# Optimization experiments

Hardware: AMD Instinct MI355X
Metric: run time of the kernel (lower is better)

Reference implementation:

```python
import jax, jax.numpy as jnp
import numpy as np
from jax import lax

B, C, D, H, W = 2, 1, 128, 128, 128
CONSCIOUSNESS_WEIGHT = 0.1


def _field(depth, height, width, dtype):
    # sin(2*pi*(d+h+w)/(D+H+W)) broadcast over batch/channel
    d = jnp.arange(depth, dtype=dtype)[:, None, None]
    h = jnp.arange(height, dtype=dtype)[None, :, None]
    w = jnp.arange(width, dtype=dtype)[None, None, :]
    phase = 2.0 * jnp.pi * (d + h + w) / (depth + height + width)
    return jnp.sin(phase)  # [D,H,W]


def _conv3d(x, w, b):
    y = lax.conv_general_dilated(
        x, w, window_strides=(1, 1, 1), padding='SAME',
        dimension_numbers=('NCDHW', 'OIDHW', 'NCDHW'))
    return y + b[None, :, None, None, None]


def setup_inputs() -> dict:
    key = jax.random.key(0)
    ks = jax.random.split(key, 4)
    fan1 = 1 * 27
    fan2 = 8 * 27
    fan3 = 16 * 27
    return {
        'cube_data': jax.random.normal(ks[0], (B, C, D, H, W), dtype=jnp.float32),
        'w1': jax.random.normal(ks[1], (8, 1, 3, 3, 3), dtype=jnp.float32) / np.sqrt(fan1),
        'b1': jnp.zeros((8,), dtype=jnp.float32),
        'w2': jax.random.normal(ks[2], (16, 8, 3, 3, 3), dtype=jnp.float32) / np.sqrt(fan2),
        'b2': jnp.zeros((16,), dtype=jnp.float32),
        'w3': jax.random.normal(ks[3], (1, 16, 3, 3, 3), dtype=jnp.float32) / np.sqrt(fan3),
        'b3': jnp.zeros((1,), dtype=jnp.float32),
    }


def reference(cube_data, w1, b1, w2, b2, w3, b3):
    _, _, d, h, w = cube_data.shape
    field = _field(d, h, w, cube_data.dtype)[None, None]  # [1,1,D,H,W]
    integrated = cube_data * (1.0 + CONSCIOUSNESS_WEIGHT * field)
    x = jax.nn.relu(_conv3d(integrated, w1, b1))
    x = jax.nn.relu(_conv3d(x, w2, b2))
    x = jnp.tanh(_conv3d(x, w3, b3))
    return x
```

## Files before the change

### kernel.cpp

```cpp
#include <hip/hip_runtime.h>
#include <hip/hip_fp16.h>

#define VOX (128 * 128 * 128)
#define P 130
#define PP (P * P)
#define PVOX (P * P * P)

typedef unsigned short u16;
typedef _Float16 f16x2 __attribute__((ext_vector_type(2)));
typedef _Float16 f16x8 __attribute__((ext_vector_type(8)));
typedef __attribute__((ext_vector_type(4))) float f32x4;
typedef __attribute__((ext_vector_type(2))) float f32x2;

__device__ __forceinline__ u16 f2h(float f) {
    return __builtin_bit_cast(unsigned short, (_Float16)f);
}
__device__ __forceinline__ unsigned pkh_relu(float a, float b) {
    float ra = a > 0.f ? a : 0.f, rb = b > 0.f ? b : 0.f;
    return (unsigned)f2h(ra) | ((unsigned)f2h(rb) << 16);
}
__device__ __forceinline__ f16x2 h2(unsigned u) { return __builtin_bit_cast(f16x2, u); }

__device__ __forceinline__ float dot2(unsigned a, unsigned b, float c) {
#if __has_builtin(__builtin_amdgcn_fdot2)
    return __builtin_amdgcn_fdot2(h2(a), h2(b), c, false);
#else
    f16x2 av = h2(a), bv = h2(b);
    c = fmaf((float)av.x, (float)bv.x, c);
    return fmaf((float)av.y, (float)bv.y, c);
#endif
}

__device__ __forceinline__ float fast_tanh(float x) {
    float e = __expf(2.0f * x);
    return 1.0f - 2.0f * __builtin_amdgcn_rcpf(1.0f + e);
}

__global__ __launch_bounds__(256) void prep_kernel(
    const float* __restrict__ w1, const float* __restrict__ w2,
    const float* __restrict__ w3, u16* __restrict__ w2frag,
    unsigned* __restrict__ w3p, float2* __restrict__ w1p) {
    int i = blockIdx.x * 256 + threadIdx.x;
    if (i < 3584) {
        int j = i & 7, l = (i >> 3) & 63, s = i >> 9;
        int tap = s * 4 + (l >> 4), oc = l & 15, ic = j;
        float v = (tap < 27) ? w2[(oc * 8 + ic) * 27 + tap] : 0.0f;
        w2frag[i] = f2h(v);
    }
    if (i < 216) {
        int tap = i >> 3, j = i & 7;
        w3p[i] = (unsigned)f2h(w3[(2 * j) * 27 + tap]) |
                 ((unsigned)f2h(w3[(2 * j + 1) * 27 + tap]) << 16);
    }
    if (i < 108) {
        int tap = i >> 2, j = i & 3;
        w1p[i] = make_float2(w1[(2 * j) * 27 + tap], w1[(2 * j + 1) * 27 + tap]);
    }
}

__global__ __launch_bounds__(256) void zero_halo_kernel(u16* __restrict__ x1,
                                                        u16* __restrict__ x2) {
    int i = blockIdx.x * 256 + threadIdx.x;
    if (i >= PVOX) return;
    int d = i / PP;
    int r = i - d * PP;
    int h = r / P;
    int w = r - h * P;
    if (d == 0 || d == P - 1 || h == 0 || h == P - 1 || w == 0 || w == P - 1) {
        uint4 z = {0u, 0u, 0u, 0u};
        *(uint4*)(x1 + (size_t)i * 8) = z;
        *(uint4*)(x2 + (size_t)i * 16) = z;
        *(uint4*)(x2 + (size_t)i * 16 + 8) = z;
    }
}

__global__ __launch_bounds__(256) void integrate_kernel(
    const float* __restrict__ in, u16* __restrict__ x0) {
    int i = blockIdx.x * 256 + threadIdx.x;
    if (i >= PVOX) return;
    int d = i / PP;
    int r = i - d * PP;
    int h = r / P;
    int w = r - h * P;
    float v = 0.0f;
    if (d >= 1 && d <= 128 && h >= 1 && h <= 128 && w >= 1 && w <= 128) {
        int s = (d - 1) + (h - 1) + (w - 1);
        float fld = 1.0f + 0.1f * sinf(6.283185307179586f * (float)s / 384.0f);
        v = in[(size_t)(d - 1) * 16384 + (h - 1) * 128 + (w - 1)] * fld;
    }
    x0[i] = f2h(v);
}

__global__ __launch_bounds__(256) void conv1_kernel(
    const u16* __restrict__ x0, const float2* __restrict__ w1p,
    const float* __restrict__ b1, u16* __restrict__ x1) {
    const int t = blockIdx.x * 256 + threadIdx.x;
    const int w0 = (t & 63) * 2;
    const int h0 = ((t >> 6) & 31) * 4;
    const int d = t >> 11;

    f32x2 acc[4][4][2];
#pragma unroll
    for (int j = 0; j < 4; ++j) {
        const f32x2 b = {b1[2 * j], b1[2 * j + 1]};
#pragma unroll
        for (int i = 0; i < 4; ++i) { acc[i][j][0] = b; acc[i][j][1] = b; }
    }

#pragma unroll
    for (int dz = 0; dz < 3; ++dz) {
        const u16* zb = x0 + (size_t)(d + dz) * PP + (size_t)h0 * P + w0;
        const float2* wz = w1p + dz * 9 * 4;
#pragma unroll
        for (int r = 0; r < 6; ++r) {
            const u16* rp = zb + r * P;
            const unsigned u0 = *(const unsigned*)rp;
            const unsigned u1 = *(const unsigned*)(rp + 2);
            float vv[4];
            vv[0] = (float)h2(u0).x; vv[1] = (float)h2(u0).y;
            vv[2] = (float)h2(u1).x; vv[3] = (float)h2(u1).y;
#pragma unroll
            for (int dy = 0; dy < 3; ++dy) {
                const int i = r - dy;
                if (i < 0 || i > 3) continue;
#pragma unroll
                for (int dx = 0; dx < 3; ++dx) {
                    const f32x2 s0 = {vv[dx], vv[dx]};
                    const f32x2 s1 = {vv[dx + 1], vv[dx + 1]};
#pragma unroll
                    for (int j = 0; j < 4; ++j) {
                        const float2 wraw = wz[(dy * 3 + dx) * 4 + j];
                        const f32x2 wv = {wraw.x, wraw.y};
                        acc[i][j][0] = __builtin_elementwise_fma(wv, s0, acc[i][j][0]);
                        acc[i][j][1] = __builtin_elementwise_fma(wv, s1, acc[i][j][1]);
                    }
                }
            }
        }
    }
    const size_t e0 = ((size_t)(d + 1) * P + (h0 + 1)) * P + (w0 + 1);
#pragma unroll
    for (int i = 0; i < 4; ++i) {
        uint4 oA, oB;
        oA.x = pkh_relu(acc[i][0][0].x, acc[i][0][0].y);
        oA.y = pkh_relu(acc[i][1][0].x, acc[i][1][0].y);
        oA.z = pkh_relu(acc[i][2][0].x, acc[i][2][0].y);
        oA.w = pkh_relu(acc[i][3][0].x, acc[i][3][0].y);
        oB.x = pkh_relu(acc[i][0][1].x, acc[i][0][1].y);
        oB.y = pkh_relu(acc[i][1][1].x, acc[i][1][1].y);
        oB.z = pkh_relu(acc[i][2][1].x, acc[i][2][1].y);
        oB.w = pkh_relu(acc[i][3][1].x, acc[i][3][1].y);
        *(uint4*)(x1 + (e0 + (size_t)i * P) * 8) = oA;
        *(uint4*)(x1 + (e0 + (size_t)i * P + 1) * 8) = oB;
    }
}

__global__ __launch_bounds__(256) void conv2_mfma_kernel(
    const u16* __restrict__ x1, const u16* __restrict__ w2frag,
    const float* __restrict__ b2, u16* __restrict__ x2) {
    const int lane = threadIdx.x & 63;
    const int row = blockIdx.x * 4 + (threadIdx.x >> 6);
    const int q = lane >> 4;
    const int mi = lane & 15;
    const int d0 = row >> 7;
    const int h0 = row & 127;

    f32x4 acc[8];
#pragma unroll
    for (int t = 0; t < 8; ++t) acc[t] = (f32x4){0.f, 0.f, 0.f, 0.f};

#pragma unroll
    for (int s = 0; s < 7; ++s) {
        int tap = s * 4 + q;
        if (tap > 26) tap = 26;
        const int dz = tap / 9;
        const int rem = tap - dz * 9;
        const int dy = rem / 3;
        const int dx = rem - dy * 3;
        const u16* bp = x1 + ((size_t)((d0 + dz) * P + (h0 + dy)) * P + (mi + dx)) * 8;
        const f16x8 wf = *(const f16x8*)(w2frag + (size_t)(s * 64 + lane) * 8);
#pragma unroll
        for (int t = 0; t < 8; ++t) {
            f16x8 act = *(const f16x8*)(bp + t * 128);
            acc[t] = __builtin_amdgcn_mfma_f32_16x16x32_f16(wf, act, acc[t], 0, 0, 0);
        }
    }

    const float4 bv = *(const float4*)(b2 + q * 4);
    const size_t obase = ((size_t)(d0 + 1) * P + (h0 + 1)) * P + 1;
#pragma unroll
    for (int t = 0; t < 8; ++t) {
        const float v0 = acc[t][0] + bv.x;
        const float v1 = acc[t][1] + bv.y;
        const float v2 = acc[t][2] + bv.z;
        const float v3 = acc[t][3] + bv.w;
        uint2 o;
        o.x = pkh_relu(v0, v1);
        o.y = pkh_relu(v2, v3);
        *(uint2*)(x2 + (obase + 16 * t + mi) * 16 + q * 4) = o;
    }
}

__global__ __launch_bounds__(256) void conv3_kernel(
    const u16* __restrict__ x2, const unsigned* __restrict__ w3p,
    const float* __restrict__ b3, float* __restrict__ out) {
    const int t = blockIdx.x * 256 + threadIdx.x;
    const int w = t & 127;
    const int h0 = ((t >> 7) & 15) * 8;
    const int d = t >> 11;

    float accA[8], accB[8];
#pragma unroll
    for (int i = 0; i < 8; ++i) { accA[i] = 0.f; accB[i] = 0.f; }

#pragma unroll 1
    for (int dz = 0; dz < 3; ++dz) {
        const u16* zb = x2 + ((size_t)((d + dz) * P + h0) * P + w) * 16;
        const unsigned* wz = w3p + dz * 9 * 8;
#pragma unroll
        for (int r = 0; r < 10; ++r) {
            const u16* rp = zb + (size_t)r * (P * 16);
            const uint4 c0l = *(const uint4*)(rp);
            const uint4 c0h = *(const uint4*)(rp + 8);
            const uint4 c1l = *(const uint4*)(rp + 16);
            const uint4 c1h = *(const uint4*)(rp + 24);
            const uint4 c2l = *(const uint4*)(rp + 32);
            const uint4 c2h = *(const uint4*)(rp + 40);
#pragma unroll
            for (int dy = 0; dy < 3; ++dy) {
                const int i = r - dy;
                if (i < 0 || i > 7) continue;
                const unsigned* wp = wz + dy * 3 * 8;
                float a = accA[i], b = accB[i];
                a = dot2(c0l.x, wp[0], a);  b = dot2(c0l.y, wp[1], b);
                a = dot2(c0l.z, wp[2], a);  b = dot2(c0l.w, wp[3], b);
                a = dot2(c0h.x, wp[4], a);  b = dot2(c0h.y, wp[5], b);
                a = dot2(c0h.z, wp[6], a);  b = dot2(c0h.w, wp[7], b);
                a = dot2(c1l.x, wp[8], a);  b = dot2(c1l.y, wp[9], b);
                a = dot2(c1l.z, wp[10], a); b = dot2(c1l.w, wp[11], b);
                a = dot2(c1h.x, wp[12], a); b = dot2(c1h.y, wp[13], b);
                a = dot2(c1h.z, wp[14], a); b = dot2(c1h.w, wp[15], b);
                a = dot2(c2l.x, wp[16], a); b = dot2(c2l.y, wp[17], b);
                a = dot2(c2l.z, wp[18], a); b = dot2(c2l.w, wp[19], b);
                a = dot2(c2h.x, wp[20], a); b = dot2(c2h.y, wp[21], b);
                a = dot2(c2h.z, wp[22], a); b = dot2(c2h.w, wp[23], b);
                accA[i] = a; accB[i] = b;
            }
        }
    }
    const float bias = b3[0];
    const size_t obase = (size_t)(d * 128 + h0) * 128 + w;
#pragma unroll
    for (int i = 0; i < 8; ++i)
        out[obase + (size_t)i * 128] = fast_tanh(accA[i] + accB[i] + bias);
}

extern "C" void kernel_launch(void* const* d_in, const int* in_sizes, int n_in,
                              void* d_out, int out_size, void* d_ws, size_t ws_size,
                              hipStream_t stream) {
    const float* cube = (const float*)d_in[0];
    const float* w1 = (const float*)d_in[1];
    const float* b1 = (const float*)d_in[2];
    const float* w2 = (const float*)d_in[3];
    const float* b2 = (const float*)d_in[4];
    const float* w3 = (const float*)d_in[5];
    const float* b3 = (const float*)d_in[6];
    float* out = (float*)d_out;

    char* ws = (char*)d_ws;
    u16* w2frag = (u16*)ws;
    unsigned* w3p = (unsigned*)(ws + 7168);
    float2* w1p = (float2*)(ws + 8032);
    u16* x0 = (u16*)(ws + 16384);
    u16* x1 = (u16*)(ws + 16384 + (size_t)PVOX * sizeof(u16));
    u16* x2 = (u16*)(ws + 16384 + (size_t)PVOX * sizeof(u16) + (size_t)PVOX * 8 * sizeof(u16));

    prep_kernel<<<dim3(14), dim3(256), 0, stream>>>(w1, w2, w3, w2frag, w3p, w1p);
    zero_halo_kernel<<<dim3((PVOX + 255) / 256), dim3(256), 0, stream>>>(x1, x2);

    for (int b = 0; b < 2; ++b) {
        integrate_kernel<<<dim3((PVOX + 255) / 256), dim3(256), 0, stream>>>(
            cube + (size_t)b * VOX, x0);
        conv1_kernel<<<dim3(VOX / 8 / 256), dim3(256), 0, stream>>>(x0, w1p, b1, x1);
        conv2_mfma_kernel<<<dim3(128 * 128 / 4), dim3(256), 0, stream>>>(x1, w2frag, b2, x2);
        conv3_kernel<<<dim3(VOX / 8 / 256), dim3(256), 0, stream>>>(
            x2, w3p, b3, out + (size_t)b * VOX);
    }
}
```

Measured before the change: 264.0 us.

## Share activation loads across dx taps in conv2 MFMA and two depths in conv3

conv2 now runs one MFMA per dx weight fragment on the same activation load, grouping the taps by (dz,dy) into 3 steps instead of 7. The dx-shifted partial sums are then combined with cross-lane shuffles, which also cuts the padded-tap waste. conv3 computes two output depth slices per thread, reusing each loaded x2 row across both, and launches half as many threads. The weight prep and halo zeroing are merged into one setup kernel, removing a launch; in exchange, conv2 needs three times as many accumulator registers plus shuffle overhead, and conv3 holds more registers per thread.

```diff
diff --git a/kernel.cpp b/kernel.cpp
--- a/kernel.cpp
+++ b/kernel.cpp
@@ -36,15 +36,18 @@
     return 1.0f - 2.0f * __builtin_amdgcn_rcpf(1.0f + e);
 }
 
-__global__ __launch_bounds__(256) void prep_kernel(
+__global__ __launch_bounds__(256) void setup_kernel(
     const float* __restrict__ w1, const float* __restrict__ w2,
     const float* __restrict__ w3, u16* __restrict__ w2frag,
-    unsigned* __restrict__ w3p, float2* __restrict__ w1p) {
+    unsigned* __restrict__ w3p, float2* __restrict__ w1p,
+    u16* __restrict__ x1, u16* __restrict__ x2) {
     int i = blockIdx.x * 256 + threadIdx.x;
-    if (i < 3584) {
-        int j = i & 7, l = (i >> 3) & 63, s = i >> 9;
-        int tap = s * 4 + (l >> 4), oc = l & 15, ic = j;
-        float v = (tap < 27) ? w2[(oc * 8 + ic) * 27 + tap] : 0.0f;
+    if (i < 4608) {
+        int j = i & 7, l = (i >> 3) & 63, g = i >> 9;
+        int s = g % 3, dx = g / 3;
+        int q = l >> 4, oc = l & 15;
+        int dzdy = s * 4 + q;
+        float v = (dzdy < 9) ? w2[(oc * 8 + j) * 27 + dzdy * 3 + dx] : 0.0f;
         w2frag[i] = f2h(v);
     }
     if (i < 216) {
@@ -56,11 +59,6 @@
         int tap = i >> 2, j = i & 3;
         w1p[i] = make_float2(w1[(2 * j) * 27 + tap], w1[(2 * j + 1) * 27 + tap]);
     }
-}
-
-__global__ __launch_bounds__(256) void zero_halo_kernel(u16* __restrict__ x1,
-                                                        u16* __restrict__ x2) {
-    int i = blockIdx.x * 256 + threadIdx.x;
     if (i >= PVOX) return;
     int d = i / PP;
     int r = i - d * PP;
@@ -165,38 +163,56 @@
     const int d0 = row >> 7;
     const int h0 = row & 127;
 
-    f32x4 acc[8];
-#pragma unroll
-    for (int t = 0; t < 8; ++t) acc[t] = (f32x4){0.f, 0.f, 0.f, 0.f};
-
-#pragma unroll
-    for (int s = 0; s < 7; ++s) {
-        int tap = s * 4 + q;
-        if (tap > 26) tap = 26;
-        const int dz = tap / 9;
-        const int rem = tap - dz * 9;
-        const int dy = rem / 3;
-        const int dx = rem - dy * 3;
-        const u16* bp = x1 + ((size_t)((d0 + dz) * P + (h0 + dy)) * P + (mi + dx)) * 8;
-        const f16x8 wf = *(const f16x8*)(w2frag + (size_t)(s * 64 + lane) * 8);
+    f32x4 acc[8][3];
+#pragma unroll
+    for (int t = 0; t < 8; ++t)
+#pragma unroll
+        for (int dx = 0; dx < 3; ++dx) acc[t][dx] = (f32x4){0.f, 0.f, 0.f, 0.f};
+
+#pragma unroll
+    for (int s = 0; s < 3; ++s) {
+        int dzdy = s * 4 + q;
+        if (dzdy > 8) dzdy = 8;
+        const int dz = dzdy / 3;
+        const int dy = dzdy - dz * 3;
+        const u16* bp = x1 + ((size_t)((d0 + dz) * P + (h0 + dy)) * P + (mi + 1)) * 8;
+        f16x8 wf[3];
+#pragma unroll
+        for (int dx = 0; dx < 3; ++dx)
+            wf[dx] = *(const f16x8*)(w2frag + (size_t)((dx * 3 + s) * 64 + lane) * 8);
+        f16x8 a[8];
+#pragma unroll
+        for (int t = 0; t < 8; ++t) a[t] = *(const f16x8*)(bp + t * 128);
 #pragma unroll
         for (int t = 0; t < 8; ++t) {
-            f16x8 act = *(const f16x8*)(bp + t * 128);
-            acc[t] = __builtin_amdgcn_mfma_f32_16x16x32_f16(wf, act, acc[t], 0, 0, 0);
+#pragma unroll
+            for (int dx = 0; dx < 3; ++dx)
+                acc[t][dx] = __builtin_amdgcn_mfma_f32_16x16x32_f16(wf[dx], a[t], acc[t][dx], 0, 0, 0);
         }
     }
 
     const float4 bv = *(const float4*)(b2 + q * 4);
     const size_t obase = ((size_t)(d0 + 1) * P + (h0 + 1)) * P + 1;
+    const int hi_lane = (lane & 48) + 15;
+    const int lo_lane = (lane & 48);
 #pragma unroll
     for (int t = 0; t < 8; ++t) {
-        const float v0 = acc[t][0] + bv.x;
-        const float v1 = acc[t][1] + bv.y;
-        const float v2 = acc[t][2] + bv.z;
-        const float v3 = acc[t][3] + bv.w;
+        const int tm = (t > 0) ? t - 1 : 0;
+        const int tp = (t < 7) ? t + 1 : 7;
+        float res[4];
+#pragma unroll
+        for (int c = 0; c < 4; ++c) {
+            const float up = __shfl_up(acc[t][0][c], 1, 16);
+            const float pu = (t > 0) ? __shfl(acc[tm][0][c], hi_lane, 64) : 0.0f;
+            const float A0 = (mi == 0) ? pu : up;
+            const float dn = __shfl_down(acc[t][2][c], 1, 16);
+            const float pd = (t < 7) ? __shfl(acc[tp][2][c], lo_lane, 64) : 0.0f;
+            const float A2 = (mi == 15) ? pd : dn;
+            res[c] = acc[t][1][c] + A0 + A2;
+        }
         uint2 o;
-        o.x = pkh_relu(v0, v1);
-        o.y = pkh_relu(v2, v3);
+        o.x = pkh_relu(res[0] + bv.x, res[1] + bv.y);
+        o.y = pkh_relu(res[2] + bv.z, res[3] + bv.w);
         *(uint2*)(x2 + (obase + 16 * t + mi) * 16 + q * 4) = o;
     }
 }
@@ -207,16 +223,17 @@
     const int t = blockIdx.x * 256 + threadIdx.x;
     const int w = t & 127;
     const int h0 = ((t >> 7) & 15) * 8;
-    const int d = t >> 11;
-
-    float accA[8], accB[8];
-#pragma unroll
-    for (int i = 0; i < 8; ++i) { accA[i] = 0.f; accB[i] = 0.f; }
+    const int d0 = (t >> 11) * 2;
+
+    float accA[2][8], accB[2][8];
+#pragma unroll
+    for (int dd = 0; dd < 2; ++dd)
+#pragma unroll
+        for (int i = 0; i < 8; ++i) { accA[dd][i] = 0.f; accB[dd][i] = 0.f; }
 
 #pragma unroll 1
-    for (int dz = 0; dz < 3; ++dz) {
-        const u16* zb = x2 + ((size_t)((d + dz) * P + h0) * P + w) * 16;
-        const unsigned* wz = w3p + dz * 9 * 8;
+    for (int z = 0; z < 4; ++z) {
+        const u16* zb = x2 + ((size_t)((d0 + z) * P + h0) * P + w) * 16;
 #pragma unroll
         for (int r = 0; r < 10; ++r) {
             const u16* rp = zb + (size_t)r * (P * 16);
@@ -227,32 +244,41 @@
             const uint4 c2l = *(const uint4*)(rp + 32);
             const uint4 c2h = *(const uint4*)(rp + 40);
 #pragma unroll
-            for (int dy = 0; dy < 3; ++dy) {
-                const int i = r - dy;
-                if (i < 0 || i > 7) continue;
-                const unsigned* wp = wz + dy * 3 * 8;
-                float a = accA[i], b = accB[i];
-                a = dot2(c0l.x, wp[0], a);  b = dot2(c0l.y, wp[1], b);
-                a = dot2(c0l.z, wp[2], a);  b = dot2(c0l.w, wp[3], b);
-                a = dot2(c0h.x, wp[4], a);  b = dot2(c0h.y, wp[5], b);
-                a = dot2(c0h.z, wp[6], a);  b = dot2(c0h.w, wp[7], b);
-                a = dot2(c1l.x, wp[8], a);  b = dot2(c1l.y, wp[9], b);
-                a = dot2(c1l.z, wp[10], a); b = dot2(c1l.w, wp[11], b);
-                a = dot2(c1h.x, wp[12], a); b = dot2(c1h.y, wp[13], b);
-                a = dot2(c1h.z, wp[14], a); b = dot2(c1h.w, wp[15], b);
-                a = dot2(c2l.x, wp[16], a); b = dot2(c2l.y, wp[17], b);
-                a = dot2(c2l.z, wp[18], a); b = dot2(c2l.w, wp[19], b);
-                a = dot2(c2h.x, wp[20], a); b = dot2(c2h.y, wp[21], b);
-                a = dot2(c2h.z, wp[22], a); b = dot2(c2h.w, wp[23], b);
-                accA[i] = a; accB[i] = b;
+            for (int dd = 0; dd < 2; ++dd) {
+                const int dz = z - dd;
+                if (dz < 0 || dz > 2) continue;
+                const unsigned* wz = w3p + dz * 9 * 8;
+#pragma unroll
+                for (int dy = 0; dy < 3; ++dy) {
+                    const int i = r - dy;
+                    if (i < 0 || i > 7) continue;
+                    const unsigned* wp = wz + dy * 3 * 8;
+                    float a = accA[dd][i], b = accB[dd][i];
+                    a = dot2(c0l.x, wp[0], a);  b = dot2(c0l.y, wp[1], b);
+                    a = dot2(c0l.z, wp[2], a);  b = dot2(c0l.w, wp[3], b);
+                    a = dot2(c0h.x, wp[4], a);  b = dot2(c0h.y, wp[5], b);
+                    a = dot2(c0h.z, wp[6], a);  b = dot2(c0h.w, wp[7], b);
+                    a = dot2(c1l.x, wp[8], a);  b = dot2(c1l.y, wp[9], b);
+                    a = dot2(c1l.z, wp[10], a); b = dot2(c1l.w, wp[11], b);
+                    a = dot2(c1h.x, wp[12], a); b = dot2(c1h.y, wp[13], b);
+                    a = dot2(c1h.z, wp[14], a); b = dot2(c1h.w, wp[15], b);
+                    a = dot2(c2l.x, wp[16], a); b = dot2(c2l.y, wp[17], b);
+                    a = dot2(c2l.z, wp[18], a); b = dot2(c2l.w, wp[19], b);
+                    a = dot2(c2h.x, wp[20], a); b = dot2(c2h.y, wp[21], b);
+                    a = dot2(c2h.z, wp[22], a); b = dot2(c2h.w, wp[23], b);
+                    accA[dd][i] = a; accB[dd][i] = b;
+                }
             }
         }
     }
     const float bias = b3[0];
-    const size_t obase = (size_t)(d * 128 + h0) * 128 + w;
-#pragma unroll
-    for (int i = 0; i < 8; ++i)
-        out[obase + (size_t)i * 128] = fast_tanh(accA[i] + accB[i] + bias);
+#pragma unroll
+    for (int dd = 0; dd < 2; ++dd) {
+        const size_t obase = (size_t)((d0 + dd) * 128 + h0) * 128 + w;
+#pragma unroll
+        for (int i = 0; i < 8; ++i)
+            out[obase + (size_t)i * 128] = fast_tanh(accA[dd][i] + accB[dd][i] + bias);
+    }
 }
 
 extern "C" void kernel_launch(void* const* d_in, const int* in_sizes, int n_in,
@@ -269,21 +295,21 @@
 
     char* ws = (char*)d_ws;
     u16* w2frag = (u16*)ws;
-    unsigned* w3p = (unsigned*)(ws + 7168);
-    float2* w1p = (float2*)(ws + 8032);
+    unsigned* w3p = (unsigned*)(ws + 9216);
+    float2* w1p = (float2*)(ws + 10080);
     u16* x0 = (u16*)(ws + 16384);
     u16* x1 = (u16*)(ws + 16384 + (size_t)PVOX * sizeof(u16));
     u16* x2 = (u16*)(ws + 16384 + (size_t)PVOX * sizeof(u16) + (size_t)PVOX * 8 * sizeof(u16));
 
-    prep_kernel<<<dim3(14), dim3(256), 0, stream>>>(w1, w2, w3, w2frag, w3p, w1p);
-    zero_halo_kernel<<<dim3((PVOX + 255) / 256), dim3(256), 0, stream>>>(x1, x2);
+    setup_kernel<<<dim3((PVOX + 255) / 256), dim3(256), 0, stream>>>(
+        w1, w2, w3, w2frag, w3p, w1p, x1, x2);
 
     for (int b = 0; b < 2; ++b) {
         integrate_kernel<<<dim3((PVOX + 255) / 256), dim3(256), 0, stream>>>(
             cube + (size_t)b * VOX, x0);
         conv1_kernel<<<dim3(VOX / 8 / 256), dim3(256), 0, stream>>>(x0, w1p, b1, x1);
         conv2_mfma_kernel<<<dim3(128 * 128 / 4), dim3(256), 0, stream>>>(x1, w2frag, b2, x2);
-        conv3_kernel<<<dim3(VOX / 8 / 256), dim3(256), 0, stream>>>(
+        conv3_kernel<<<dim3(VOX / 16 / 256), dim3(256), 0, stream>>>(
             x2, w3p, b3, out + (size_t)b * VOX);
     }
 }
```

After: 267.0 us. Within noise of the previous version (+1.1%).

## Stage conv2 input rows in LDS, block conv3 over two depths, merge setup kernels

Applied to the files above, without the earlier changes.

conv2 now gives each block 4 adjacent h-rows at one depth. It cooperatively loads the 18 needed padded input rows into shared memory and preloads all weight fragments into registers, so the MFMA loop reads activations from LDS instead of global memory. conv3 computes two output depth slices per thread and reuses each loaded input plane for both, which cuts its global loads. The weight-prep and halo-zeroing kernels are merged into one launch. The cost is shared-memory use and a barrier in conv2, and more accumulator registers in conv3, both of which may lower occupancy.

```diff
diff --git a/kernel.cpp b/kernel.cpp
--- a/kernel.cpp
+++ b/kernel.cpp
@@ -5,6 +5,8 @@
 #define P 130
 #define PP (P * P)
 #define PVOX (P * P * P)
+#define LROW 130
+#define NR 18
 
 typedef unsigned short u16;
 typedef _Float16 f16x2 __attribute__((ext_vector_type(2)));
@@ -36,15 +38,16 @@
     return 1.0f - 2.0f * __builtin_amdgcn_rcpf(1.0f + e);
 }
 
-__global__ __launch_bounds__(256) void prep_kernel(
+__global__ __launch_bounds__(256) void setup_kernel(
     const float* __restrict__ w1, const float* __restrict__ w2,
     const float* __restrict__ w3, u16* __restrict__ w2frag,
-    unsigned* __restrict__ w3p, float2* __restrict__ w1p) {
+    unsigned* __restrict__ w3p, float2* __restrict__ w1p,
+    u16* __restrict__ x1, u16* __restrict__ x2) {
     int i = blockIdx.x * 256 + threadIdx.x;
     if (i < 3584) {
         int j = i & 7, l = (i >> 3) & 63, s = i >> 9;
-        int tap = s * 4 + (l >> 4), oc = l & 15, ic = j;
-        float v = (tap < 27) ? w2[(oc * 8 + ic) * 27 + tap] : 0.0f;
+        int tap = s * 4 + (l >> 4), oc = l & 15;
+        float v = (tap < 27) ? w2[(oc * 8 + j) * 27 + tap] : 0.0f;
         w2frag[i] = f2h(v);
     }
     if (i < 216) {
@@ -56,11 +59,6 @@
         int tap = i >> 2, j = i & 3;
         w1p[i] = make_float2(w1[(2 * j) * 27 + tap], w1[(2 * j + 1) * 27 + tap]);
     }
-}
-
-__global__ __launch_bounds__(256) void zero_halo_kernel(u16* __restrict__ x1,
-                                                        u16* __restrict__ x2) {
-    int i = blockIdx.x * 256 + threadIdx.x;
     if (i >= PVOX) return;
     int d = i / PP;
     int r = i - d * PP;
@@ -158,12 +156,31 @@
 __global__ __launch_bounds__(256) void conv2_mfma_kernel(
     const u16* __restrict__ x1, const u16* __restrict__ w2frag,
     const float* __restrict__ b2, u16* __restrict__ x2) {
-    const int lane = threadIdx.x & 63;
-    const int row = blockIdx.x * 4 + (threadIdx.x >> 6);
+    __shared__ u16 sm[NR * LROW * 8];
+
+    const int tid = threadIdx.x;
+    const int lane = tid & 63;
+    const int wv = tid >> 6;
     const int q = lane >> 4;
     const int mi = lane & 15;
-    const int d0 = row >> 7;
-    const int h0 = row & 127;
+    const int d0 = blockIdx.x >> 5;
+    const int h0 = (blockIdx.x & 31) * 4;
+
+    for (int u = tid; u < NR * LROW; u += 256) {
+        const int row = u / LROW;
+        const int pos = u - row * LROW;
+        const int dz = row / 6;
+        const int r = row - dz * 6;
+        const uint4 v = *(const uint4*)(x1 + ((size_t)((d0 + dz) * P + (h0 + r)) * P + pos) * 8);
+        *(uint4*)(sm + (size_t)u * 8) = v;
+    }
+
+    f16x8 wf[7];
+#pragma unroll
+    for (int s = 0; s < 7; ++s)
+        wf[s] = *(const f16x8*)(w2frag + (size_t)(s * 64 + lane) * 8);
+
+    __syncthreads();
 
     f32x4 acc[8];
 #pragma unroll
@@ -177,26 +194,21 @@
         const int rem = tap - dz * 9;
         const int dy = rem / 3;
         const int dx = rem - dy * 3;
-        const u16* bp = x1 + ((size_t)((d0 + dz) * P + (h0 + dy)) * P + (mi + dx)) * 8;
-        const f16x8 wf = *(const f16x8*)(w2frag + (size_t)(s * 64 + lane) * 8);
+        const u16* bp = sm + ((dz * 6 + wv + dy) * LROW + (mi + dx)) * 8;
 #pragma unroll
         for (int t = 0; t < 8; ++t) {
             f16x8 act = *(const f16x8*)(bp + t * 128);
-            acc[t] = __builtin_amdgcn_mfma_f32_16x16x32_f16(wf, act, acc[t], 0, 0, 0);
+            acc[t] = __builtin_amdgcn_mfma_f32_16x16x32_f16(wf[s], act, acc[t], 0, 0, 0);
         }
     }
 
     const float4 bv = *(const float4*)(b2 + q * 4);
-    const size_t obase = ((size_t)(d0 + 1) * P + (h0 + 1)) * P + 1;
+    const size_t obase = ((size_t)(d0 + 1) * P + (h0 + wv + 1)) * P + 1;
 #pragma unroll
     for (int t = 0; t < 8; ++t) {
-        const float v0 = acc[t][0] + bv.x;
-        const float v1 = acc[t][1] + bv.y;
-        const float v2 = acc[t][2] + bv.z;
-        const float v3 = acc[t][3] + bv.w;
         uint2 o;
-        o.x = pkh_relu(v0, v1);
-        o.y = pkh_relu(v2, v3);
+        o.x = pkh_relu(acc[t][0] + bv.x, acc[t][1] + bv.y);
+        o.y = pkh_relu(acc[t][2] + bv.z, acc[t][3] + bv.w);
         *(uint2*)(x2 + (obase + 16 * t + mi) * 16 + q * 4) = o;
     }
 }
@@ -207,16 +219,17 @@
     const int t = blockIdx.x * 256 + threadIdx.x;
     const int w = t & 127;
     const int h0 = ((t >> 7) & 15) * 8;
-    const int d = t >> 11;
-
-    float accA[8], accB[8];
-#pragma unroll
-    for (int i = 0; i < 8; ++i) { accA[i] = 0.f; accB[i] = 0.f; }
+    const int d0 = (t >> 11) * 2;
+
+    float accA[2][8], accB[2][8];
+#pragma unroll
+    for (int dd = 0; dd < 2; ++dd)
+#pragma unroll
+        for (int i = 0; i < 8; ++i) { accA[dd][i] = 0.f; accB[dd][i] = 0.f; }
 
 #pragma unroll 1
-    for (int dz = 0; dz < 3; ++dz) {
-        const u16* zb = x2 + ((size_t)((d + dz) * P + h0) * P + w) * 16;
-        const unsigned* wz = w3p + dz * 9 * 8;
+    for (int z = 0; z < 4; ++z) {
+        const u16* zb = x2 + ((size_t)((d0 + z) * P + h0) * P + w) * 16;
 #pragma unroll
         for (int r = 0; r < 10; ++r) {
             const u16* rp = zb + (size_t)r * (P * 16);
@@ -227,32 +240,41 @@
             const uint4 c2l = *(const uint4*)(rp + 32);
             const uint4 c2h = *(const uint4*)(rp + 40);
 #pragma unroll
-            for (int dy = 0; dy < 3; ++dy) {
-                const int i = r - dy;
-                if (i < 0 || i > 7) continue;
-                const unsigned* wp = wz + dy * 3 * 8;
-                float a = accA[i], b = accB[i];
-                a = dot2(c0l.x, wp[0], a);  b = dot2(c0l.y, wp[1], b);
-                a = dot2(c0l.z, wp[2], a);  b = dot2(c0l.w, wp[3], b);
-                a = dot2(c0h.x, wp[4], a);  b = dot2(c0h.y, wp[5], b);
-                a = dot2(c0h.z, wp[6], a);  b = dot2(c0h.w, wp[7], b);
-                a = dot2(c1l.x, wp[8], a);  b = dot2(c1l.y, wp[9], b);
-                a = dot2(c1l.z, wp[10], a); b = dot2(c1l.w, wp[11], b);
-                a = dot2(c1h.x, wp[12], a); b = dot2(c1h.y, wp[13], b);
-                a = dot2(c1h.z, wp[14], a); b = dot2(c1h.w, wp[15], b);
-                a = dot2(c2l.x, wp[16], a); b = dot2(c2l.y, wp[17], b);
-                a = dot2(c2l.z, wp[18], a); b = dot2(c2l.w, wp[19], b);
-                a = dot2(c2h.x, wp[20], a); b = dot2(c2h.y, wp[21], b);
-                a = dot2(c2h.z, wp[22], a); b = dot2(c2h.w, wp[23], b);
-                accA[i] = a; accB[i] = b;
+            for (int dd = 0; dd < 2; ++dd) {
+                const int dz = z - dd;
+                if (dz < 0 || dz > 2) continue;
+                const unsigned* wz = w3p + dz * 9 * 8;
+#pragma unroll
+                for (int dy = 0; dy < 3; ++dy) {
+                    const int i = r - dy;
+                    if (i < 0 || i > 7) continue;
+                    const unsigned* wp = wz + dy * 3 * 8;
+                    float a = accA[dd][i], b = accB[dd][i];
+                    a = dot2(c0l.x, wp[0], a);  b = dot2(c0l.y, wp[1], b);
+                    a = dot2(c0l.z, wp[2], a);  b = dot2(c0l.w, wp[3], b);
+                    a = dot2(c0h.x, wp[4], a);  b = dot2(c0h.y, wp[5], b);
+                    a = dot2(c0h.z, wp[6], a);  b = dot2(c0h.w, wp[7], b);
+                    a = dot2(c1l.x, wp[8], a);  b = dot2(c1l.y, wp[9], b);
+                    a = dot2(c1l.z, wp[10], a); b = dot2(c1l.w, wp[11], b);
+                    a = dot2(c1h.x, wp[12], a); b = dot2(c1h.y, wp[13], b);
+                    a = dot2(c1h.z, wp[14], a); b = dot2(c1h.w, wp[15], b);
+                    a = dot2(c2l.x, wp[16], a); b = dot2(c2l.y, wp[17], b);
+                    a = dot2(c2l.z, wp[18], a); b = dot2(c2l.w, wp[19], b);
+                    a = dot2(c2h.x, wp[20], a); b = dot2(c2h.y, wp[21], b);
+                    a = dot2(c2h.z, wp[22], a); b = dot2(c2h.w, wp[23], b);
+                    accA[dd][i] = a; accB[dd][i] = b;
+                }
             }
         }
     }
     const float bias = b3[0];
-    const size_t obase = (size_t)(d * 128 + h0) * 128 + w;
-#pragma unroll
-    for (int i = 0; i < 8; ++i)
-        out[obase + (size_t)i * 128] = fast_tanh(accA[i] + accB[i] + bias);
+#pragma unroll
+    for (int dd = 0; dd < 2; ++dd) {
+        const size_t obase = (size_t)((d0 + dd) * 128 + h0) * 128 + w;
+#pragma unroll
+        for (int i = 0; i < 8; ++i)
+            out[obase + (size_t)i * 128] = fast_tanh(accA[dd][i] + accB[dd][i] + bias);
+    }
 }
 
 extern "C" void kernel_launch(void* const* d_in, const int* in_sizes, int n_in,
@@ -275,15 +297,15 @@
     u16* x1 = (u16*)(ws + 16384 + (size_t)PVOX * sizeof(u16));
     u16* x2 = (u16*)(ws + 16384 + (size_t)PVOX * sizeof(u16) + (size_t)PVOX * 8 * sizeof(u16));
 
-    prep_kernel<<<dim3(14), dim3(256), 0, stream>>>(w1, w2, w3, w2frag, w3p, w1p);
-    zero_halo_kernel<<<dim3((PVOX + 255) / 256), dim3(256), 0, stream>>>(x1, x2);
+    setup_kernel<<<dim3((PVOX + 255) / 256), dim3(256), 0, stream>>>(
+        w1, w2, w3, w2frag, w3p, w1p, x1, x2);
 
     for (int b = 0; b < 2; ++b) {
         integrate_kernel<<<dim3((PVOX + 255) / 256), dim3(256), 0, stream>>>(
             cube + (size_t)b * VOX, x0);
         conv1_kernel<<<dim3(VOX / 8 / 256), dim3(256), 0, stream>>>(x0, w1p, b1, x1);
-        conv2_mfma_kernel<<<dim3(128 * 128 / 4), dim3(256), 0, stream>>>(x1, w2frag, b2, x2);
-        conv3_kernel<<<dim3(VOX / 8 / 256), dim3(256), 0, stream>>>(
+        conv2_mfma_kernel<<<dim3(128 * 32), dim3(256), 0, stream>>>(x1, w2frag, b2, x2);
+        conv3_kernel<<<dim3(VOX / 16 / 256), dim3(256), 0, stream>>>(
             x2, w3p, b3, out + (size_t)b * VOX);
     }
 }
```

New measurement: 249.6 us. -5.5%, faster.
